# Performance work log

Hardware: AMD Instinct MI355X
Metric: run time of the kernel (lower is better)

Reference implementation:

```python
import jax, jax.numpy as jnp
import numpy as np

NUM_NEURONS = 256
NUM_SAMPLES = 512
MAX_SPIKES = 32
N_STEPS = 32          # fixed RK4 steps per spike round (stands in for adaptive Tsit5)
ALPHA = 0.03
V_RESET = 1.0
T0 = 0.0


def setup_inputs() -> dict:
    key = jax.random.key(0)
    ks = jax.random.split(key, 7)
    input_current = jax.random.normal(ks[0], (NUM_NEURONS,), dtype=jnp.float32)
    # _build_w with network=all-False: uniform(minval=0.5), mask sets nothing
    w = jax.random.uniform(ks[1], (NUM_NEURONS, NUM_NEURONS), minval=0.5, maxval=1.0, dtype=jnp.float32)
    mu = jax.random.uniform(ks[2], (2,), minval=0.5, maxval=1.0, dtype=jnp.float32)
    v0 = jax.random.normal(ks[3], (NUM_NEURONS,), dtype=jnp.float32)
    i0 = jax.random.normal(ks[4], (NUM_NEURONS,), dtype=jnp.float32)
    # s0 = log(U) - alpha  (always < 0)
    s0 = (jnp.log(jax.random.uniform(ks[5], (NUM_SAMPLES, NUM_NEURONS), minval=1e-6, maxval=1.0)) - ALPHA).astype(jnp.float32)
    # pre-drawn stochastic resets, one per (spike round, sample, neuron)
    reset_s = (jnp.log(jax.random.uniform(ks[6], (MAX_SPIKES, NUM_SAMPLES, NUM_NEURONS), minval=1e-6, maxval=1.0)) - ALPHA).astype(jnp.float32)
    return dict(input_current=input_current, w=w, mu=mu, v0=v0, i0=i0, s0=s0, reset_s=reset_s, t1=2)


def _drift(y, ic, mu1, mu2):
    # y: [samples, neurons, 3] = (v, i, s)
    v, i = y[..., 0], y[..., 1]
    dv = mu1 * (i + ic - v)
    di = -mu2 * i
    ds = jax.nn.sigmoid(v)  # intensity_fn(v)
    return jnp.stack([dv, di, ds], axis=-1)


def reference(input_current, w, mu, v0, i0, s0, reset_s, t1):
    t1f = jnp.float32(t1)
    mu1, mu2 = mu[0], mu[1]
    ic = input_current  # constant-in-time input current, [neurons]

    y0 = jnp.concatenate([
        jnp.broadcast_to(v0, (NUM_SAMPLES, NUM_NEURONS))[..., None],
        jnp.broadcast_to(i0, (NUM_SAMPLES, NUM_NEURONS))[..., None],
        s0[..., None]], axis=-1)  # [samples, neurons, 3]

    def rk4(y, h):
        k1 = _drift(y, ic, mu1, mu2)
        k2 = _drift(y + 0.5 * h * k1, ic, mu1, mu2)
        k3 = _drift(y + 0.5 * h * k2, ic, mu1, mu2)
        k4 = _drift(y + h * k3, ic, mu1, mu2)
        return y + (h / 6.0) * (k1 + 2.0 * k2 + 2.0 * k3 + k4)

    def round_body(carry, reset_k):
        t0s, y_in = carry                      # t0s: [samples]
        dt = (t1f - t0s) / N_STEPS             # per-sample step size
        h = dt[:, None, None]

        def step(sc, _):
            t, y, done, tev, yev, emask = sc
            y_new = rk4(y, h)
            y_new = jnp.where(done[:, None, None], y, y_new)  # freeze after event
            s_prev, s_new = y[..., 2], y_new[..., 2]
            crossed = s_new > 0.0                              # cond_fn root: s crosses 0
            trig = crossed.any(axis=1) & (~done)
            idx = jnp.argmax(s_new, axis=1)                    # event neuron (first/largest crossing)
            sp = jnp.take_along_axis(s_prev, idx[:, None], 1)[:, 0]
            sn = jnp.take_along_axis(s_new, idx[:, None], 1)[:, 0]
            frac = jnp.clip(sp / (sp - sn + 1e-12), 0.0, 1.0)  # linear root estimate (Newton stand-in)
            t_c = t + frac * dt
            y_c = y + frac[:, None, None] * (y_new - y)
            tev = jnp.where(trig, t_c, tev)
            yev = jnp.where(trig[:, None, None], y_c, yev)
            emask = jnp.where(trig[:, None], crossed, emask)
            y = jnp.where(trig[:, None, None], y_c, y_new)
            done = done | trig
            return (t + dt, y, done, tev, yev, emask), None

        done0 = jnp.zeros((NUM_SAMPLES,), bool)
        tev0 = jnp.full((NUM_SAMPLES,), jnp.inf, jnp.float32)
        em0 = jnp.zeros((NUM_SAMPLES, NUM_NEURONS), bool)
        (_, yend, done, tev, yev, emask), _ = jax.lax.scan(
            step, (t0s, y_in, done0, tev0, y_in, em0), None, length=N_STEPS)

        tev = jnp.where(done, tev, t1f)                 # no event -> sol.ts[-1] = t1
        yev = jnp.where(done[:, None, None], yev, yend)

        # trans_fn: spike reset + synaptic jump w[event_idx]
        eidx = jnp.argmax(emask, axis=1)
        w_row = jnp.where(done[:, None], w[eidx], 0.0)  # zero if no event happened
        v_t = yev[..., 0] - jnp.where(emask, V_RESET, 0.0)
        i_t = yev[..., 1] + w_row
        s_t = jnp.minimum(jnp.where(emask, reset_k, yev[..., 2]), 0.0)
        y_next = jnp.stack([v_t, i_t, s_t], axis=-1)
        return (tev, y_next), (tev, yev, emask)

    t0s = jnp.full((NUM_SAMPLES,), T0, jnp.float32)
    _, (tevs, yevs, emasks) = jax.lax.scan(jax.checkpoint(round_body), (t0s, y0), reset_s)

    spike_times = jnp.transpose(tevs, (1, 0))            # [samples, max_spikes]
    spike_values = jnp.transpose(yevs, (1, 0, 2, 3))     # [samples, max_spikes, neurons, 3]
    spike_marks = jnp.transpose(emasks, (1, 0, 2))       # [samples, max_spikes, neurons]
    return spike_times, spike_values, spike_marks
```

## Files before the change

kernel.cpp:

```cpp
#include <hip/hip_runtime.h>
#include <math.h>

#define NN 256
#define NS 512
#define MS 32
#define NSTEP 32
#define VRESET 1.0f

__device__ __forceinline__ float sigf(float x) {
    float e = __expf(-x);
    return __builtin_amdgcn_rcpf(1.0f + e);
}

__global__ __launch_bounds__(256) void snn_kernel(
    const float* __restrict__ ic_g,
    const float* __restrict__ w,
    const float* __restrict__ mu,
    const float* __restrict__ v0,
    const float* __restrict__ i0,
    const float* __restrict__ s0,
    const float* __restrict__ reset_s,
    const int*   __restrict__ t1p,
    float* __restrict__ out)
{
    const int tid  = threadIdx.x;
    const int lane = tid & 63;
    const int wid  = tid >> 6;
    const int samp = blockIdx.x;
    const float mu1 = mu[0];
    const float mu2 = mu[1];
    const float t1f = (float)t1p[0];

    __shared__ int   s_any[2][4];
    __shared__ float s_bv[4], s_bsp[4];
    __shared__ int   s_bn[4];
    __shared__ int   s_eidx[4];

    float v  = v0[tid];
    float ii = i0[tid];
    float s  = s0[samp * NN + tid];
    const float ic = ic_g[tid];
    float t0 = 0.0f;

    float* times = out;
    float* vals  = out + (size_t)NS * MS;
    float* marks = out + (size_t)NS * MS * (1 + NN * 3);

    for (int r = 0; r < MS; ++r) {
        const float dt = (t1f - t0) / (float)NSTEP;
        float tev = t1f;
        float yev_v, yev_i, yev_s;
        bool  em = false;
        bool  done = false;

        if (dt != 0.0f) {
            float t = t0;
            const float hh = 0.5f * dt;
            const float h6 = dt * (1.0f / 6.0f);
            for (int st = 0; st < NSTEP; ++st) {
                float kv1 = mu1 * (ii + ic - v);
                float ki1 = -mu2 * ii;
                float ks1 = sigf(v);
                float v2 = v + hh * kv1;
                float i2 = ii + hh * ki1;
                float kv2 = mu1 * (i2 + ic - v2);
                float ki2 = -mu2 * i2;
                float ks2 = sigf(v2);
                float v3 = v + hh * kv2;
                float i3 = ii + hh * ki2;
                float kv3 = mu1 * (i3 + ic - v3);
                float ki3 = -mu2 * i3;
                float ks3 = sigf(v3);
                float v4 = v + dt * kv3;
                float i4 = ii + dt * ki3;
                float kv4 = mu1 * (i4 + ic - v4);
                float ki4 = -mu2 * i4;
                float ks4 = sigf(v4);
                float vn = v  + h6 * (kv1 + 2.0f * kv2 + 2.0f * kv3 + kv4);
                float in_ = ii + h6 * (ki1 + 2.0f * ki2 + 2.0f * ki3 + ki4);
                float sn = s  + h6 * (ks1 + 2.0f * ks2 + 2.0f * ks3 + ks4);

                unsigned long long bl = __ballot(sn > 0.0f);
                if (lane == 0) s_any[st & 1][wid] = (bl != 0ull) ? 1 : 0;
                __syncthreads();
                int anyflag = s_any[st & 1][0] | s_any[st & 1][1] |
                              s_any[st & 1][2] | s_any[st & 1][3];

                if (anyflag) {
                    float bv = sn, bsp = s;
                    int   bn = tid;
#pragma unroll
                    for (int off = 32; off >= 1; off >>= 1) {
                        float ov  = __shfl_xor(bv, off);
                        float osp = __shfl_xor(bsp, off);
                        int   on  = __shfl_xor(bn, off);
                        if (ov > bv || (ov == bv && on < bn)) { bv = ov; bsp = osp; bn = on; }
                    }
                    if (lane == 0) { s_bv[wid] = bv; s_bsp[wid] = bsp; s_bn[wid] = bn; }
                    __syncthreads();
                    bv = s_bv[0]; bsp = s_bsp[0]; bn = s_bn[0];
#pragma unroll
                    for (int wv = 1; wv < 4; ++wv) {
                        float ov = s_bv[wv], osp = s_bsp[wv];
                        int   on = s_bn[wv];
                        if (ov > bv || (ov == bv && on < bn)) { bv = ov; bsp = osp; bn = on; }
                    }
                    float frac = bsp / (bsp - bv + 1e-12f);
                    frac = fminf(fmaxf(frac, 0.0f), 1.0f);
                    tev = t + frac * dt;
                    yev_v = v  + frac * (vn - v);
                    yev_i = ii + frac * (in_ - ii);
                    yev_s = s  + frac * (sn - s);
                    em = sn > 0.0f;
                    v = yev_v; ii = yev_i; s = yev_s;
                    done = true;
                    break;
                }
                v = vn; ii = in_; s = sn;
                t += dt;
            }
        }

        if (!done) {
            tev = t1f;
            yev_v = v; yev_i = ii; yev_s = s; em = false;
        }

        const int sr = samp * MS + r;
        if (tid == 0) times[sr] = tev;
        {
            float* p = vals + ((size_t)sr * NN + tid) * 3;
            p[0] = yev_v;
            p[1] = yev_i;
            p[2] = yev_s;
            marks[(size_t)sr * NN + tid] = em ? 1.0f : 0.0f;
        }

        if (done) {
            unsigned long long bm = __ballot(em);
            int cand = (bm != 0ull) ? (wid * 64 + (int)__builtin_ctzll(bm)) : (2 * NN);
            if (lane == 0) s_eidx[wid] = cand;
            __syncthreads();
            int eidx = s_eidx[0];
            eidx = (s_eidx[1] < eidx) ? s_eidx[1] : eidx;
            eidx = (s_eidx[2] < eidx) ? s_eidx[2] : eidx;
            eidx = (s_eidx[3] < eidx) ? s_eidx[3] : eidx;

            float wr = w[eidx * NN + tid];
            v  = yev_v - (em ? VRESET : 0.0f);
            ii = yev_i + wr;
            float sres = em ? reset_s[((size_t)r * NS + samp) * NN + tid] : yev_s;
            s = fminf(sres, 0.0f);
        } else {
            s = fminf(s, 0.0f);
        }
        t0 = tev;
    }
}

extern "C" void kernel_launch(void* const* d_in, const int* in_sizes, int n_in,
                              void* d_out, int out_size, void* d_ws, size_t ws_size,
                              hipStream_t stream) {
    const float* ic      = (const float*)d_in[0];
    const float* w       = (const float*)d_in[1];
    const float* mu      = (const float*)d_in[2];
    const float* v0      = (const float*)d_in[3];
    const float* i0      = (const float*)d_in[4];
    const float* s0      = (const float*)d_in[5];
    const float* reset_s = (const float*)d_in[6];
    const int*   t1p     = (const int*)d_in[7];
    float* out = (float*)d_out;

    snn_kernel<<<dim3(NS), dim3(256), 0, stream>>>(ic, w, mu, v0, i0, s0,
                                                   reset_s, t1p, out);
}
```

Before: 153.0 us.

## Collapse linear RK4 v/i update into precomputed affine coefficients per round

Because the v and i drift is linear, each RK4 step is rewritten as a fixed affine map whose coefficients are computed once per spike round in double precision. Only the sigmoid stages need their own arguments, each formed from a couple of FMAs. The loop is also restructured so the any-flag check happens at the top of the next iteration, which shortens the dependent chain before the barrier. This costs some per-round double-precision setup and can change float rounding compared with the stage-by-stage evaluation.

```diff
diff --git a/kernel.cpp b/kernel.cpp
--- a/kernel.cpp
+++ b/kernel.cpp
@@ -27,8 +27,8 @@
     const int lane = tid & 63;
     const int wid  = tid >> 6;
     const int samp = blockIdx.x;
-    const float mu1 = mu[0];
-    const float mu2 = mu[1];
+    const double m1d = (double)mu[0];
+    const double m2d = (double)mu[1];
     const float t1f = (float)t1p[0];
 
     __shared__ int   s_any[2][4];
@@ -54,70 +54,92 @@
         bool  done = false;
 
         if (dt != 0.0f) {
-            float t = t0;
-            const float hh = 0.5f * dt;
+            const double hd = (double)dt;
+            const double a  = hd * m1d;
+            const double b  = hd * m2d;
+            const double p2 = 1.0 - 0.5 * a, q2 = 0.5 * a, r2 = 0.5 * a;
+            const double i2c = 1.0 - 0.5 * b;
+            const double p3 = 1.0 - 0.5 * a * p2;
+            const double q3 = 0.5 * a * (i2c - q2);
+            const double r3 = 0.5 * a * (1.0 - r2);
+            const double i3c = 1.0 - 0.5 * b * i2c;
+            const double p4 = 1.0 - a * p3;
+            const double q4 = a * (i3c - q3);
+            const double r4 = a * (1.0 - r3);
+            const double i4c = 1.0 - b * i3c;
+            const double a6 = a / 6.0, b6 = b / 6.0;
+            const float fR00 = (float)(1.0 - a6 * (1.0 + 2.0 * p2 + 2.0 * p3 + p4));
+            const float fR01 = (float)(a6 * (1.0 + 2.0 * (i2c - q2) + 2.0 * (i3c - q3) + (i4c - q4)));
+            const float fC0  = (float)(a6 * (1.0 + 2.0 * (1.0 - r2) + 2.0 * (1.0 - r3) + (1.0 - r4)));
+            const float fR11 = (float)(1.0 - b6 * (1.0 + 2.0 * i2c + 2.0 * i3c + i4c));
+            const float fp2 = (float)p2, fq2 = (float)q2;
+            const float fp3 = (float)p3, fq3 = (float)q3;
+            const float fp4 = (float)p4, fq4 = (float)q4;
+            const float r2ic = (float)r2 * ic;
+            const float r3ic = (float)r3 * ic;
+            const float r4ic = (float)r4 * ic;
+            const float c0ic = fC0 * ic;
             const float h6 = dt * (1.0f / 6.0f);
-            for (int st = 0; st < NSTEP; ++st) {
-                float kv1 = mu1 * (ii + ic - v);
-                float ki1 = -mu2 * ii;
-                float ks1 = sigf(v);
-                float v2 = v + hh * kv1;
-                float i2 = ii + hh * ki1;
-                float kv2 = mu1 * (i2 + ic - v2);
-                float ki2 = -mu2 * i2;
-                float ks2 = sigf(v2);
-                float v3 = v + hh * kv2;
-                float i3 = ii + hh * ki2;
-                float kv3 = mu1 * (i3 + ic - v3);
-                float ki3 = -mu2 * i3;
-                float ks3 = sigf(v3);
-                float v4 = v + dt * kv3;
-                float i4 = ii + dt * ki3;
-                float kv4 = mu1 * (i4 + ic - v4);
-                float ki4 = -mu2 * i4;
-                float ks4 = sigf(v4);
-                float vn = v  + h6 * (kv1 + 2.0f * kv2 + 2.0f * kv3 + kv4);
-                float in_ = ii + h6 * (ki1 + 2.0f * ki2 + 2.0f * ki3 + ki4);
-                float sn = s  + h6 * (ks1 + 2.0f * ks2 + 2.0f * ks3 + ks4);
 
-                unsigned long long bl = __ballot(sn > 0.0f);
+            float t = t0, tprev = t0;
+            float vp = v, ip = ii, sp = s;
+
+            for (int st = 0; st <= NSTEP; ++st) {
+                if (st > 0) {
+                    int anyflag = s_any[(st - 1) & 1][0] | s_any[(st - 1) & 1][1] |
+                                  s_any[(st - 1) & 1][2] | s_any[(st - 1) & 1][3];
+                    if (anyflag) {
+                        float bv = s, bsp = sp;
+                        int   bn = tid;
+#pragma unroll
+                        for (int off = 32; off >= 1; off >>= 1) {
+                            float ov  = __shfl_xor(bv, off);
+                            float osp = __shfl_xor(bsp, off);
+                            int   on  = __shfl_xor(bn, off);
+                            if (ov > bv || (ov == bv && on < bn)) { bv = ov; bsp = osp; bn = on; }
+                        }
+                        if (lane == 0) { s_bv[wid] = bv; s_bsp[wid] = bsp; s_bn[wid] = bn; }
+                        __syncthreads();
+                        bv = s_bv[0]; bsp = s_bsp[0]; bn = s_bn[0];
+#pragma unroll
+                        for (int wv = 1; wv < 4; ++wv) {
+                            float ov = s_bv[wv], osp = s_bsp[wv];
+                            int   on = s_bn[wv];
+                            if (ov > bv || (ov == bv && on < bn)) { bv = ov; bsp = osp; bn = on; }
+                        }
+                        float frac = bsp / (bsp - bv + 1e-12f);
+                        frac = fminf(fmaxf(frac, 0.0f), 1.0f);
+                        tev = tprev + frac * dt;
+                        yev_v = vp + frac * (v  - vp);
+                        yev_i = ip + frac * (ii - ip);
+                        yev_s = sp + frac * (s  - sp);
+                        em = s > 0.0f;
+                        v = yev_v; ii = yev_i; s = yev_s;
+                        done = true;
+                        break;
+                    }
+                }
+                if (st == NSTEP) break;
+
+                vp = v; ip = ii; sp = s; tprev = t;
+                float a2 = fmaf(fp2, vp, fmaf(fq2, ip, r2ic));
+                float a3 = fmaf(fp3, vp, fmaf(fq3, ip, r3ic));
+                float a4 = fmaf(fp4, vp, fmaf(fq4, ip, r4ic));
+                float k1 = sigf(vp);
+                float k2 = sigf(a2);
+                float k3 = sigf(a3);
+                float k4 = sigf(a4);
+                v  = fmaf(fR00, vp, fmaf(fR01, ip, c0ic));
+                ii = fR11 * ip;
+                float ts = fmaf(2.0f, k2, k1);
+                ts = fmaf(2.0f, k3, ts);
+                ts = ts + k4;
+                s = fmaf(h6, ts, sp);
+
+                unsigned long long bl = __ballot(s > 0.0f);
                 if (lane == 0) s_any[st & 1][wid] = (bl != 0ull) ? 1 : 0;
+                t = tprev + dt;
                 __syncthreads();
-                int anyflag = s_any[st & 1][0] | s_any[st & 1][1] |
-                              s_any[st & 1][2] | s_any[st & 1][3];
-
-                if (anyflag) {
-                    float bv = sn, bsp = s;
-                    int   bn = tid;
-#pragma unroll
-                    for (int off = 32; off >= 1; off >>= 1) {
-                        float ov  = __shfl_xor(bv, off);
-                        float osp = __shfl_xor(bsp, off);
-                        int   on  = __shfl_xor(bn, off);
-                        if (ov > bv || (ov == bv && on < bn)) { bv = ov; bsp = osp; bn = on; }
-                    }
-                    if (lane == 0) { s_bv[wid] = bv; s_bsp[wid] = bsp; s_bn[wid] = bn; }
-                    __syncthreads();
-                    bv = s_bv[0]; bsp = s_bsp[0]; bn = s_bn[0];
-#pragma unroll
-                    for (int wv = 1; wv < 4; ++wv) {
-                        float ov = s_bv[wv], osp = s_bsp[wv];
-                        int   on = s_bn[wv];
-                        if (ov > bv || (ov == bv && on < bn)) { bv = ov; bsp = osp; bn = on; }
-                    }
-                    float frac = bsp / (bsp - bv + 1e-12f);
-                    frac = fminf(fmaxf(frac, 0.0f), 1.0f);
-                    tev = t + frac * dt;
-                    yev_v = v  + frac * (vn - v);
-                    yev_i = ii + frac * (in_ - ii);
-                    yev_s = s  + frac * (sn - s);
-                    em = sn > 0.0f;
-                    v = yev_v; ii = yev_i; s = yev_s;
-                    done = true;
-                    break;
-                }
-                v = vn; ii = in_; s = sn;
-                t += dt;
             }
         }
 
```

Result: slower. 158.1 us (+3.3%).
